# Performance work log

Hardware: AMD Instinct MI355X
Metric: run time of the kernel (lower is better)

Reference implementation:

```python
import jax, jax.numpy as jnp
import numpy as np

B, S, D = 4, 2048, 1024
H = 2 * D          # hidden_dim = 2*n_embd
A = H // 16        # adapt_dim
E = 8              # num_experts
GS = 4             # group_size
G = E // GS        # num_groups
K = 2              # top-k experts within group


def _ln(x, g, b, eps=1e-5):
    m = x.mean(-1, keepdims=True)
    v = ((x - m) ** 2).mean(-1, keepdims=True)
    return (x - m) * jax.lax.rsqrt(v + eps) * g + b


def setup_inputs() -> dict:
    key = jax.random.key(0)
    ks = jax.random.split(key, 14)
    n = lambda k, shape, s: jax.random.normal(k, shape, jnp.float32) * s
    sc = 1.0 / float(np.sqrt(D))
    asc = 0.01 / float(np.sqrt(A))
    return {
        'x': n(ks[0], (B, S, D), 1.0),
        'Wu': n(ks[1], (H, D), sc),        # shared_up
        'Wg': n(ks[2], (H, D), sc),        # shared_gate
        'Wd': n(ks[3], (D, H), sc),        # shared_down
        'Wpre': n(ks[4], (A, D), sc * 0.01),   # pre_adapt
        'Wpost': n(ks[5], (A, H), sc * 0.01),  # post_adapt
        'ln_g': jnp.ones((A,), jnp.float32),
        'ln_b': jnp.zeros((A,), jnp.float32),
        'Wap': n(ks[6], (H, A), sc * 0.01),    # adapt_proj
        'Wea': n(ks[7], (E, A, A), asc),       # per-expert adapter linears
        'ln_eg': jnp.ones((E, A), jnp.float32),
        'ln_eb': jnp.zeros((E, A), jnp.float32),
        'Wep': n(ks[8], (H, A), asc),          # expert_proj
        'Wop': n(ks[9], (D, H), asc),          # output_proj
        'Wgr': n(ks[10], (G, D), 0.001),       # router_group
        'Wer': n(ks[11], (GS, D), 0.001),      # router_expert
    }


def _forward(x, Wu, Wg, Wd, Wpre, Wpost, ln_g, ln_b, Wap, Wea, ln_eg, ln_eb, Wep, Wop, Wgr, Wer):
    N = B * S
    xf = x.reshape(N, D)
    # --- hierarchical router ---
    gl = xf @ Wgr.T                              # [N,G]
    gp = jax.nn.softmax(gl, axis=-1)
    gw, gi = jax.lax.top_k(gp, 1)                # top-1 group
    el = xf @ Wer.T                              # [N,GS]
    ep = jax.nn.softmax(el, axis=-1)
    lw, li = jax.lax.top_k(ep, K)                # top-k local experts
    lw = lw / (lw.sum(-1, keepdims=True) + 1e-7)
    fw = gw * lw                                 # [N,K] final weights
    idx = gi * GS + li                           # [N,K] global expert ids (distinct per token)
    dispatch = jnp.zeros((N, E), x.dtype).at[jnp.arange(N)[:, None], idx].set(fw)
    load = dispatch.sum(0)
    target = load.sum() / E
    rloss = 0.001 * (jnp.mean((load - target) ** 2) + jnp.mean(gl ** 2) + jnp.mean(el ** 2))
    # --- shared expert MLP ---
    hidden = jax.nn.silu(x @ Wg.T) * (x @ Wu.T)  # [B,S,H]
    ai = _ln(x @ Wpre.T, ln_g, ln_b)             # [B,S,A]
    ao = _ln(hidden @ Wpost.T, ln_g, ln_b)       # [B,S,A]
    aw = jax.nn.silu(jnp.clip(jnp.einsum('bsa,bta->bst', ai, ao), -5.0, 5.0))  # [B,S,S]
    adapt = jnp.einsum('bst,bta->bsa', aw, ai) @ Wap.T
    hidden = hidden + 0.1 * adapt
    shared = hidden @ Wd.T                       # [B,S,D]
    # --- expert group (dense form of masked gather/scatter; w==0 off-mask) ---
    w = dispatch.reshape(B, S, E)
    h0 = x @ Wpre.T                              # [B,S,A]
    he = _ln(jnp.einsum('bsa,eca->bsec', h0, Wea), ln_eg, ln_eb)  # [B,S,E,A]
    M = Wop @ Wep                                # output_proj o expert_proj, [D,A]
    out = shared * w.sum(-1, keepdims=True) + 0.1 * jnp.einsum('bsec,bse,dc->bsd', he, w, M)
    return out, rloss


def reference(x, Wu, Wg, Wd, Wpre, Wpost, ln_g, ln_b, Wap, Wea, ln_eg, ln_eb, Wep, Wop, Wgr, Wer):
    return _forward(x, Wu, Wg, Wd, Wpre, Wpost, ln_g, ln_b, Wap, Wea, ln_eg, ln_eb, Wep, Wop, Wgr, Wer)
```

## Files before the change

### kernel.cpp

```cpp
#include <hip/hip_runtime.h>
#include <math.h>


typedef __bf16 bf16_t;
typedef __attribute__((ext_vector_type(8))) __bf16 bf16x8;
typedef __attribute__((ext_vector_type(4))) float f32x4;

__device__ __forceinline__ float b2f(bf16_t v) { return (float)v; }
__device__ __forceinline__ bf16_t f2b(float v) { return (bf16_t)v; }
__device__ __forceinline__ float siluf(float v) { return v / (1.f + expf(-v)); }

static constexpr int Bb = 4, S = 2048, D = 1024, H = 2048, A = 128, E = 8;
static constexpr int N = Bb * S;

typedef __attribute__((address_space(1))) void gvoid;
typedef __attribute__((address_space(3))) void svoid;
__device__ __forceinline__ void gll16(const bf16_t* g, bf16_t* l) {
  __builtin_amdgcn_global_load_lds((gvoid*)g, (svoid*)l, 16, 0, 0);
}

__device__ __forceinline__ long tidx(int row, int k, int K, int lgTR) {
  int TRm = (1 << lgTR) - 1;
  int q = (k >> 3) & 3;
  int p = q ^ (row & 3);
  return ((((long)(row >> lgTR) * (K >> 5) + (k >> 5)) << lgTR) + (row & TRm)) * 32 +
         ((long)p << 3);
}

__device__ __forceinline__ bf16x8 ld8f(const float* p) {
  float4 a = *reinterpret_cast<const float4*>(p);
  float4 b = *reinterpret_cast<const float4*>(p + 4);
  bf16x8 r;
  r[0] = f2b(a.x); r[1] = f2b(a.y); r[2] = f2b(a.z); r[3] = f2b(a.w);
  r[4] = f2b(b.x); r[5] = f2b(b.y); r[6] = f2b(b.z); r[7] = f2b(b.w);
  return r;
}
__device__ __forceinline__ void split8(const float* p, bf16x8& h, bf16x8& l) {
  float4 a = *reinterpret_cast<const float4*>(p);
  float4 b = *reinterpret_cast<const float4*>(p + 4);
  float v[8] = {a.x, a.y, a.z, a.w, b.x, b.y, b.z, b.w};
#pragma unroll
  for (int j = 0; j < 8; j++) {
    bf16_t hh = f2b(v[j]);
    h[j] = hh;
    l[j] = f2b(v[j] - b2f(hh));
  }
}
__device__ __forceinline__ bf16x8 ld8m(const void* p, int row, int k, int K, int m) {
  if (m == 1) return ld8f(reinterpret_cast<const float*>(p) + (long)row * K + k);
  if (m == 2)
    return *reinterpret_cast<const bf16x8*>(
        reinterpret_cast<const bf16_t*>(p) + tidx(row, k, K, 7));
  return *reinterpret_cast<const bf16x8*>(
      reinterpret_cast<const bf16_t*>(p) + (long)row * K + k);
}

template <int LGTR, int LGNKS>
__global__ __launch_bounds__(256) void split_tiled(
    const float* __restrict__ in, bf16_t* __restrict__ hi,
    bf16_t* __restrict__ lo, long total, int K) {
  long stride = (long)gridDim.x * 256;
  for (long o = (long)blockIdx.x * 256 + threadIdx.x; o < total; o += stride) {
    int p = (int)(o & 3);
    long t = o >> 2;
    int r = (int)(t & ((1 << LGTR) - 1));
    long t2 = t >> LGTR;
    int ks = (int)(t2 & ((1 << LGNKS) - 1));
    long rt = t2 >> LGNKS;
    long row = (rt << LGTR) + r;
    int k = (ks << 5) + ((p ^ (r & 3)) << 3);
    bf16x8 h, l;
    split8(in + row * K + k, h, l);
    reinterpret_cast<bf16x8*>(hi)[o] = h;
    reinterpret_cast<bf16x8*>(lo)[o] = l;
  }
}

template <int WM, int WN, int MODE>
__global__ __launch_bounds__(256) void gemm_nt_b(
    const void* __restrict__ Ag, const void* __restrict__ Bg,
    void* __restrict__ Cv, void* __restrict__ Cv2, int M, int Nn, int K,
    const float* __restrict__ aux, int aF, int bF) {
  constexpr int BM = 2 * WM, BN = 2 * WN, AM = WM / 16, AN = WN / 16;
  constexpr int LDT = 40;
  __shared__ alignas(16) bf16_t As[BM * LDT];
  __shared__ alignas(16) bf16_t Bs[BN * LDT];

  const int tid = threadIdx.x;
  const int wave = tid >> 6, lane = tid & 63;
  const int wr = wave >> 1, wc = wave & 1;
  const int quad = lane >> 4, l16 = lane & 15;
  const int rowA0 = blockIdx.y * BM, rowB0 = blockIdx.x * BN;

  f32x4 acc[AM][AN] = {};

  for (int k0 = 0; k0 < K; k0 += 32) {
    for (int c = tid; c < BM * 4; c += 256) {
      int r = c >> 2, kc = c & 3;
      *reinterpret_cast<bf16x8*>(&As[r * LDT + kc * 8]) =
          ld8m(Ag, rowA0 + r, k0 + kc * 8, K, aF);
    }
    for (int c = tid; c < BN * 4; c += 256) {
      int r = c >> 2, kc = c & 3;
      *reinterpret_cast<bf16x8*>(&Bs[r * LDT + kc * 8]) =
          ld8m(Bg, rowB0 + r, k0 + kc * 8, K, bF);
    }
    __syncthreads();
    bf16x8 af[AM], bfv[AN];
#pragma unroll
    for (int i = 0; i < AM; i++)
      af[i] = *reinterpret_cast<bf16x8*>(&As[(wr * WM + i * 16 + l16) * LDT + quad * 8]);
#pragma unroll
    for (int j = 0; j < AN; j++)
      bfv[j] = *reinterpret_cast<bf16x8*>(&Bs[(wc * WN + j * 16 + l16) * LDT + quad * 8]);
#pragma unroll
    for (int i = 0; i < AM; i++)
#pragma unroll
      for (int j = 0; j < AN; j++)
        acc[i][j] = __builtin_amdgcn_mfma_f32_16x16x32_bf16(af[i], bfv[j], acc[i][j], 0, 0, 0);
    __syncthreads();
  }

#pragma unroll
  for (int i = 0; i < AM; i++)
#pragma unroll
    for (int j = 0; j < AN; j++)
#pragma unroll
      for (int r = 0; r < 4; r++) {
        int row = rowA0 + wr * WM + i * 16 + quad * 4 + r;
        int col = rowB0 + wc * WN + j * 16 + l16;
        float v = acc[i][j][r];
        if constexpr (MODE == 0) {
          reinterpret_cast<bf16_t*>(Cv)[(long)row * Nn + col] = f2b(v);
        } else if constexpr (MODE == 1) {
          v = fminf(fmaxf(v, -5.f), 5.f);
          reinterpret_cast<bf16_t*>(Cv)[(long)row * Nn + col] = f2b(siluf(v));
        } else if constexpr (MODE == 2) {
          float* C = reinterpret_cast<float*>(Cv);
          long o = (long)row * Nn + col;
          C[o] = C[o] + 0.1f * v;
        } else if constexpr (MODE == 3) {
          float* C = reinterpret_cast<float*>(Cv);
          long o = (long)row * Nn + col;
          C[o] = C[o] * aux[row] + 0.1f * v;
        } else {
          bf16_t* Ch = reinterpret_cast<bf16_t*>(Cv);
          bf16_t* Cl = reinterpret_cast<bf16_t*>(Cv2);
          long o = tidx(row, col, Nn, 7) + (col & 7);
          float s = b2f(Ch[o]) + b2f(Cl[o]) + 0.1f * v;
          bf16_t hh = f2b(s);
          Ch[o] = hh;
          Cl[o] = f2b(s - b2f(hh));
        }
      }
}

__global__ __launch_bounds__(256) void gemm_gu_g(
    const bf16_t* __restrict__ xhT, const bf16_t* __restrict__ xlT,
    const bf16_t* __restrict__ WghT, const bf16_t* __restrict__ WglT,
    const bf16_t* __restrict__ WuhT, const bf16_t* __restrict__ WulT,
    bf16_t* __restrict__ Hh, bf16_t* __restrict__ Hl) {
  __shared__ alignas(16) bf16_t Ah[128 * 32];
  __shared__ alignas(16) bf16_t Al[128 * 32];
  __shared__ alignas(16) bf16_t B1h[64 * 32];
  __shared__ alignas(16) bf16_t B1l[64 * 32];
  __shared__ alignas(16) bf16_t B2h[64 * 32];
  __shared__ alignas(16) bf16_t B2l[64 * 32];

  const int tid = threadIdx.x;
  const int wave = tid >> 6, lane = tid & 63;
  const int wr = wave >> 1, wc = wave & 1;
  const int quad = lane >> 4, l16 = lane & 15;
  const int sw = (quad ^ (l16 & 3)) << 3;
  const int bm = blockIdx.y, bn = blockIdx.x;
  constexpr int nks = D / 32;

  f32x4 ag[4][2] = {}, au[4][2] = {};

  for (int ks = 0; ks < nks; ks++) {
    const int wo = wave << 9;
    long ao = (((long)bm * nks + ks) << 12) + wo + lane * 8;
    long bo = (((long)bn * nks + ks) << 11) + wo + lane * 8;
    gll16(xhT + ao, Ah + wo);
    gll16(xhT + ao + 2048, Ah + wo + 2048);
    gll16(xlT + ao, Al + wo);
    gll16(xlT + ao + 2048, Al + wo + 2048);
    gll16(WghT + bo, B1h + wo);
    gll16(WglT + bo, B1l + wo);
    gll16(WuhT + bo, B2h + wo);
    gll16(WulT + bo, B2l + wo);
    __syncthreads();
    bf16x8 afh[4], afl[4], b1h[2], b1l[2], b2h[2], b2l[2];
#pragma unroll
    for (int i = 0; i < 4; i++) {
      int ro = (wr * 64 + i * 16 + l16) * 32 + sw;
      afh[i] = *reinterpret_cast<bf16x8*>(&Ah[ro]);
      afl[i] = *reinterpret_cast<bf16x8*>(&Al[ro]);
    }
#pragma unroll
    for (int j = 0; j < 2; j++) {
      int ro = (wc * 32 + j * 16 + l16) * 32 + sw;
      b1h[j] = *reinterpret_cast<bf16x8*>(&B1h[ro]);
      b1l[j] = *reinterpret_cast<bf16x8*>(&B1l[ro]);
      b2h[j] = *reinterpret_cast<bf16x8*>(&B2h[ro]);
      b2l[j] = *reinterpret_cast<bf16x8*>(&B2l[ro]);
    }
#pragma unroll
    for (int i = 0; i < 4; i++)
#pragma unroll
      for (int j = 0; j < 2; j++) {
        ag[i][j] = __builtin_amdgcn_mfma_f32_16x16x32_bf16(afh[i], b1h[j], ag[i][j], 0, 0, 0);
        ag[i][j] = __builtin_amdgcn_mfma_f32_16x16x32_bf16(afh[i], b1l[j], ag[i][j], 0, 0, 0);
        ag[i][j] = __builtin_amdgcn_mfma_f32_16x16x32_bf16(afl[i], b1h[j], ag[i][j], 0, 0, 0);
        au[i][j] = __builtin_amdgcn_mfma_f32_16x16x32_bf16(afh[i], b2h[j], au[i][j], 0, 0, 0);
        au[i][j] = __builtin_amdgcn_mfma_f32_16x16x32_bf16(afh[i], b2l[j], au[i][j], 0, 0, 0);
        au[i][j] = __builtin_amdgcn_mfma_f32_16x16x32_bf16(afl[i], b2h[j], au[i][j], 0, 0, 0);
      }
    __syncthreads();
  }

#pragma unroll
  for (int i = 0; i < 4; i++)
#pragma unroll
    for (int j = 0; j < 2; j++)
#pragma unroll
      for (int r = 0; r < 4; r++) {
        int row = bm * 128 + wr * 64 + i * 16 + quad * 4 + r;
        int col = bn * 64 + wc * 32 + j * 16 + l16;
        long o = tidx(row, col, H, 7) + (col & 7);
        float v = siluf(ag[i][j][r]) * au[i][j][r];
        bf16_t hh = f2b(v);
        Hh[o] = hh;
        Hl[o] = f2b(v - b2f(hh));
      }
}

__global__ __launch_bounds__(256) void gemm_dn_g(
    const bf16_t* __restrict__ HhT, const bf16_t* __restrict__ HlT,
    const bf16_t* __restrict__ WdhT, const bf16_t* __restrict__ WdlT,
    float* __restrict__ Cg) {
  __shared__ alignas(16) bf16_t Ah[128 * 32];
  __shared__ alignas(16) bf16_t Al[128 * 32];
  __shared__ alignas(16) bf16_t Bh[128 * 32];
  __shared__ alignas(16) bf16_t Bl[128 * 32];

  const int tid = threadIdx.x;
  const int wave = tid >> 6, lane = tid & 63;
  const int wr = wave >> 1, wc = wave & 1;
  const int quad = lane >> 4, l16 = lane & 15;
  const int sw = (quad ^ (l16 & 3)) << 3;
  const int by = blockIdx.y, bx = blockIdx.x;
  constexpr int nks = H / 32;

  f32x4 acc[4][4] = {};

  for (int ks = 0; ks < nks; ks++) {
    const int wo = wave << 9;
    long ao = (((long)by * nks + ks) << 12) + wo + lane * 8;
    long bo = (((long)bx * nks + ks) << 12) + wo + lane * 8;
    gll16(HhT + ao, Ah + wo);
    gll16(HhT + ao + 2048, Ah + wo + 2048);
    gll16(HlT + ao, Al + wo);
    gll16(HlT + ao + 2048, Al + wo + 2048);
    gll16(WdhT + bo, Bh + wo);
    gll16(WdhT + bo + 2048, Bh + wo + 2048);
    gll16(WdlT + bo, Bl + wo);
    gll16(WdlT + bo + 2048, Bl + wo + 2048);
    __syncthreads();
    bf16x8 afh[4], afl[4], bfh[4], bfl[4];
#pragma unroll
    for (int i = 0; i < 4; i++) {
      int ro = (wr * 64 + i * 16 + l16) * 32 + sw;
      afh[i] = *reinterpret_cast<bf16x8*>(&Ah[ro]);
      afl[i] = *reinterpret_cast<bf16x8*>(&Al[ro]);
    }
#pragma unroll
    for (int j = 0; j < 4; j++) {
      int ro = (wc * 64 + j * 16 + l16) * 32 + sw;
      bfh[j] = *reinterpret_cast<bf16x8*>(&Bh[ro]);
      bfl[j] = *reinterpret_cast<bf16x8*>(&Bl[ro]);
    }
#pragma unroll
    for (int i = 0; i < 4; i++)
#pragma unroll
      for (int j = 0; j < 4; j++) {
        acc[i][j] = __builtin_amdgcn_mfma_f32_16x16x32_bf16(afh[i], bfh[j], acc[i][j], 0, 0, 0);
        acc[i][j] = __builtin_amdgcn_mfma_f32_16x16x32_bf16(afh[i], bfl[j], acc[i][j], 0, 0, 0);
        acc[i][j] = __builtin_amdgcn_mfma_f32_16x16x32_bf16(afl[i], bfh[j], acc[i][j], 0, 0, 0);
      }
    __syncthreads();
  }

#pragma unroll
  for (int i = 0; i < 4; i++)
#pragma unroll
    for (int j = 0; j < 4; j++)
#pragma unroll
      for (int r = 0; r < 4; r++) {
        int row = by * 128 + wr * 64 + i * 16 + quad * 4 + r;
        int col = bx * 128 + wc * 64 + j * 16 + l16;
        Cg[(long)row * D + col] = acc[i][j][r];
      }
}

__global__ __launch_bounds__(256) void fused_adapt(
    const bf16_t* __restrict__ aib, const bf16_t* __restrict__ aob,
    const bf16_t* __restrict__ aiT, bf16_t* __restrict__ adpre) {
  constexpr int LDQ = 136;
  constexpr int LDP = 72;
  __shared__ alignas(16) bf16_t Qs[64 * LDQ];
  __shared__ alignas(16) bf16_t Os[64 * LDQ];
  __shared__ alignas(16) bf16_t Ps[64 * LDP];
  __shared__ alignas(16) bf16_t Vs[128 * LDP];

  const int tid = threadIdx.x;
  const int wave = tid >> 6, lane = tid & 63;
  const int wr = wave >> 1, wc = wave & 1;
  const int quad = lane >> 4, l16 = lane & 15;
  const int b = blockIdx.y;
  const int q0 = blockIdx.x * 64;

  for (int c = tid; c < 1024; c += 256) {
    int r = c >> 4, cc = c & 15;
    *reinterpret_cast<bf16x8*>(&Qs[r * LDQ + cc * 8]) =
        *reinterpret_cast<const bf16x8*>(&aib[((long)b * S + q0 + r) * A + cc * 8]);
  }

  f32x4 o[2][4] = {};

  for (int tt = 0; tt < S / 64; tt++) {
    const int t0 = tt * 64;
    __syncthreads();
    for (int c = tid; c < 1024; c += 256) {
      int r = c >> 4, cc = c & 15;
      *reinterpret_cast<bf16x8*>(&Os[r * LDQ + cc * 8]) =
          *reinterpret_cast<const bf16x8*>(&aob[((long)b * S + t0 + r) * A + cc * 8]);
    }
    for (int c = tid; c < 1024; c += 256) {
      int r = c >> 3, cc = c & 7;
      *reinterpret_cast<bf16x8*>(&Vs[r * LDP + cc * 8]) =
          *reinterpret_cast<const bf16x8*>(&aiT[((long)b * A + r) * S + t0 + cc * 8]);
    }
    __syncthreads();
    f32x4 p[2][2] = {};
#pragma unroll
    for (int ks = 0; ks < 4; ks++) {
      bf16x8 af[2], bfv[2];
#pragma unroll
      for (int i = 0; i < 2; i++)
        af[i] = *reinterpret_cast<bf16x8*>(&Qs[(wr * 32 + i * 16 + l16) * LDQ + ks * 32 + quad * 8]);
#pragma unroll
      for (int j = 0; j < 2; j++)
        bfv[j] = *reinterpret_cast<bf16x8*>(&Os[(wc * 32 + j * 16 + l16) * LDQ + ks * 32 + quad * 8]);
#pragma unroll
      for (int i = 0; i < 2; i++)
#pragma unroll
        for (int j = 0; j < 2; j++)
          p[i][j] = __builtin_amdgcn_mfma_f32_16x16x32_bf16(af[i], bfv[j], p[i][j], 0, 0, 0);
    }
#pragma unroll
    for (int i = 0; i < 2; i++)
#pragma unroll
      for (int j = 0; j < 2; j++)
#pragma unroll
        for (int r = 0; r < 4; r++) {
          int row = wr * 32 + i * 16 + quad * 4 + r;
          int col = wc * 32 + j * 16 + l16;
          float v = fminf(fmaxf(p[i][j][r], -5.f), 5.f);
          Ps[row * LDP + col] = f2b(siluf(v));
        }
    __syncthreads();
#pragma unroll
    for (int ks = 0; ks < 2; ks++) {
      bf16x8 paf[2], vbf[4];
#pragma unroll
      for (int i = 0; i < 2; i++)
        paf[i] = *reinterpret_cast<bf16x8*>(&Ps[(wr * 32 + i * 16 + l16) * LDP + ks * 32 + quad * 8]);
#pragma unroll
      for (int j = 0; j < 4; j++)
        vbf[j] = *reinterpret_cast<bf16x8*>(&Vs[(wc * 64 + j * 16 + l16) * LDP + ks * 32 + quad * 8]);
#pragma unroll
      for (int i = 0; i < 2; i++)
#pragma unroll
        for (int j = 0; j < 4; j++)
          o[i][j] = __builtin_amdgcn_mfma_f32_16x16x32_bf16(paf[i], vbf[j], o[i][j], 0, 0, 0);
    }
  }

#pragma unroll
  for (int i = 0; i < 2; i++)
#pragma unroll
    for (int j = 0; j < 4; j++)
#pragma unroll
      for (int r = 0; r < 4; r++) {
        int row = q0 + wr * 32 + i * 16 + quad * 4 + r;
        int col = wc * 64 + j * 16 + l16;
        adpre[((long)b * S + row) * A + col] = f2b(o[i][j][r]);
      }
}

__global__ __launch_bounds__(256) void gemm_mb_splitk(
    const float* __restrict__ Ag, const bf16_t* __restrict__ Bg,
    float* __restrict__ Mp, int M, int Nn, int K) {
  constexpr int BM = 64, BN = 64, LDT = 40;
  __shared__ alignas(16) bf16_t As[BM * LDT];
  __shared__ alignas(16) bf16_t Bs[BN * LDT];
  const int tid = threadIdx.x;
  const int wave = tid >> 6, lane = tid & 63;
  const int wr = wave >> 1, wc = wave & 1;
  const int quad = lane >> 4, l16 = lane & 15;
  const int rowA0 = blockIdx.y * BM, rowB0 = blockIdx.x * BN;
  const int kz = blockIdx.z;
  const int ks0 = kz * (K / 8), ks1 = ks0 + K / 8;

  f32x4 acc[2][2] = {};
  for (int k0 = ks0; k0 < ks1; k0 += 32) {
    for (int c = tid; c < BM * 4; c += 256) {
      int r = c >> 2, kc = c & 3;
      *reinterpret_cast<bf16x8*>(&As[r * LDT + kc * 8]) =
          ld8f(Ag + (long)(rowA0 + r) * K + k0 + kc * 8);
    }
    for (int c = tid; c < BN * 4; c += 256) {
      int r = c >> 2, kc = c & 3;
      *reinterpret_cast<bf16x8*>(&Bs[r * LDT + kc * 8]) =
          *reinterpret_cast<const bf16x8*>(&Bg[(long)(rowB0 + r) * K + k0 + kc * 8]);
    }
    __syncthreads();
    bf16x8 af[2], bfv[2];
#pragma unroll
    for (int i = 0; i < 2; i++)
      af[i] = *reinterpret_cast<bf16x8*>(&As[(wr * 32 + i * 16 + l16) * LDT + quad * 8]);
#pragma unroll
    for (int j = 0; j < 2; j++)
      bfv[j] = *reinterpret_cast<bf16x8*>(&Bs[(wc * 32 + j * 16 + l16) * LDT + quad * 8]);
#pragma unroll
    for (int i = 0; i < 2; i++)
#pragma unroll
      for (int j = 0; j < 2; j++)
        acc[i][j] = __builtin_amdgcn_mfma_f32_16x16x32_bf16(af[i], bfv[j], acc[i][j], 0, 0, 0);
    __syncthreads();
  }
#pragma unroll
  for (int i = 0; i < 2; i++)
#pragma unroll
    for (int j = 0; j < 2; j++)
#pragma unroll
      for (int r = 0; r < 4; r++) {
        int row = rowA0 + wr * 32 + i * 16 + quad * 4 + r;
        int col = rowB0 + wc * 32 + j * 16 + l16;
        Mp[(long)kz * M * Nn + (long)row * Nn + col] = acc[i][j][r];
      }
}

__global__ __launch_bounds__(256) void mb_combine(
    const float* __restrict__ Mp, bf16_t* __restrict__ Mb, int total) {
  int i = blockIdx.x * 256 + threadIdx.x;
  if (i >= total) return;
  float s = 0.f;
#pragma unroll
  for (int z = 0; z < 8; z++) s += Mp[(long)z * total + i];
  Mb[i] = f2b(s);
}

__global__ __launch_bounds__(256) void gemm_dn_hl(
    const float* __restrict__ Ag, const float* __restrict__ Bg,
    float* __restrict__ Cg, int M, int Nn, int K) {
  constexpr int BM = 128, BN = 128, LDT = 40;
  __shared__ alignas(16) bf16_t Ah[BM * LDT];
  __shared__ alignas(16) bf16_t Al[BM * LDT];
  __shared__ alignas(16) bf16_t Bh[BN * LDT];
  __shared__ alignas(16) bf16_t Bl[BN * LDT];

  const int tid = threadIdx.x;
  const int wave = tid >> 6, lane = tid & 63;
  const int wr = wave >> 1, wc = wave & 1;
  const int quad = lane >> 4, l16 = lane & 15;
  const int rowA0 = blockIdx.y * BM, rowB0 = blockIdx.x * BN;

  f32x4 acc[4][4] = {};

  for (int k0 = 0; k0 < K; k0 += 32) {
    for (int c = tid; c < BM * 4; c += 256) {
      int r = c >> 2, kc = c & 3;
      bf16x8 h, l;
      split8(&Ag[(long)(rowA0 + r) * K + k0 + kc * 8], h, l);
      *reinterpret_cast<bf16x8*>(&Ah[r * LDT + kc * 8]) = h;
      *reinterpret_cast<bf16x8*>(&Al[r * LDT + kc * 8]) = l;
    }
    for (int c = tid; c < BN * 4; c += 256) {
      int r = c >> 2, kc = c & 3;
      bf16x8 h, l;
      split8(&Bg[(long)(rowB0 + r) * K + k0 + kc * 8], h, l);
      *reinterpret_cast<bf16x8*>(&Bh[r * LDT + kc * 8]) = h;
      *reinterpret_cast<bf16x8*>(&Bl[r * LDT + kc * 8]) = l;
    }
    __syncthreads();
    bf16x8 afh[4], afl[4], bfh[4], bfl[4];
#pragma unroll
    for (int i = 0; i < 4; i++) {
      int ro = (wr * 64 + i * 16 + l16) * LDT + quad * 8;
      afh[i] = *reinterpret_cast<bf16x8*>(&Ah[ro]);
      afl[i] = *reinterpret_cast<bf16x8*>(&Al[ro]);
    }
#pragma unroll
    for (int j = 0; j < 4; j++) {
      int ro = (wc * 64 + j * 16 + l16) * LDT + quad * 8;
      bfh[j] = *reinterpret_cast<bf16x8*>(&Bh[ro]);
      bfl[j] = *reinterpret_cast<bf16x8*>(&Bl[ro]);
    }
#pragma unroll
    for (int i = 0; i < 4; i++)
#pragma unroll
      for (int j = 0; j < 4; j++) {
        acc[i][j] = __builtin_amdgcn_mfma_f32_16x16x32_bf16(afh[i], bfh[j], acc[i][j], 0, 0, 0);
        acc[i][j] = __builtin_amdgcn_mfma_f32_16x16x32_bf16(afh[i], bfl[j], acc[i][j], 0, 0, 0);
        acc[i][j] = __builtin_amdgcn_mfma_f32_16x16x32_bf16(afl[i], bfh[j], acc[i][j], 0, 0, 0);
      }
    __syncthreads();
  }

#pragma unroll
  for (int i = 0; i < 4; i++)
#pragma unroll
    for (int j = 0; j < 4; j++)
#pragma unroll
      for (int r = 0; r < 4; r++) {
        int row = rowA0 + wr * 64 + i * 16 + quad * 4 + r;
        int col = rowB0 + wc * 64 + j * 16 + l16;
        Cg[(long)row * Nn + col] = acc[i][j][r];
      }
}

__global__ __launch_bounds__(256) void gemm_gu_hl(
    const float* __restrict__ x, const float* __restrict__ Wg,
    const float* __restrict__ Wu, float* __restrict__ Cg, int M, int Nn, int K) {
  constexpr int BM = 128, BN = 64, LDT = 40;
  __shared__ alignas(16) bf16_t Ah[BM * LDT];
  __shared__ alignas(16) bf16_t Al[BM * LDT];
  __shared__ alignas(16) bf16_t B1h[BN * LDT];
  __shared__ alignas(16) bf16_t B1l[BN * LDT];
  __shared__ alignas(16) bf16_t B2h[BN * LDT];
  __shared__ alignas(16) bf16_t B2l[BN * LDT];

  const int tid = threadIdx.x;
// ... 95 lines not shown
    float mg = fmaxf(gl0, gl1);
    float e0 = expf(gl0 - mg), e1 = expf(gl1 - mg);
    float inv = 1.f / (e0 + e1);
    float gp0 = e0 * inv, gp1 = e1 * inv;
    int gi = (gp1 > gp0) ? 1 : 0;
    float gw = gi ? gp1 : gp0;
    float el[4] = {dots[2], dots[3], dots[4], dots[5]};
    float me = fmaxf(fmaxf(el[0], el[1]), fmaxf(el[2], el[3]));
    float ep[4], es = 0.f;
#pragma unroll
    for (int j = 0; j < 4; j++) { ep[j] = expf(el[j] - me); es += ep[j]; }
    float inve = 1.f / es;
#pragma unroll
    for (int j = 0; j < 4; j++) ep[j] *= inve;
    int i1 = 0;
    for (int j = 1; j < 4; j++) if (ep[j] > ep[i1]) i1 = j;
    int i2 = (i1 == 0) ? 1 : 0;
    for (int j = 0; j < 4; j++) if (j != i1 && j != i2 && ep[j] > ep[i2]) i2 = j;
    float l1 = ep[i1], l2 = ep[i2];
    float ils = 1.f / (l1 + l2 + 1e-7f);
    float f1 = gw * l1 * ils, f2 = gw * l2 * ils;
    eidx[token * 2] = gi * 4 + i1;
    eidx[token * 2 + 1] = gi * 4 + i2;
    fw[token * 2] = f1;
    fw[token * 2 + 1] = f2;
    wsum[token] = f1 + f2;
    part[wv][gi * 4 + i1] = f1;
    part[wv][gi * 4 + i2] = f2;
    part[wv][8] = gl0 * gl0 + gl1 * gl1;
    part[wv][9] = el[0] * el[0] + el[1] * el[1] + el[2] * el[2] + el[3] * el[3];
  }
  __syncthreads();
  if (threadIdx.x < 12) {
    lpart[(long)blockIdx.x * 12 + threadIdx.x] =
        part[0][threadIdx.x] + part[1][threadIdx.x] +
        part[2][threadIdx.x] + part[3][threadIdx.x];
  }
}

__global__ __launch_bounds__(256) void ln_rows(
    const bf16_t* __restrict__ in, const float* __restrict__ g,
    const float* __restrict__ b, bf16_t* __restrict__ out) {
  const int row = blockIdx.x * 4 + (threadIdx.x >> 6);
  const int lane = threadIdx.x & 63;
  const bf16_t* p = in + (long)row * A;
  float x0 = b2f(p[lane]), x1 = b2f(p[lane + 64]);
  float s = x0 + x1;
#pragma unroll
  for (int off = 32; off; off >>= 1) s += __shfl_xor(s, off);
  float mean = s * (1.f / 128.f);
  float d0 = x0 - mean, d1 = x1 - mean;
  float q = d0 * d0 + d1 * d1;
#pragma unroll
  for (int off = 32; off; off >>= 1) q += __shfl_xor(q, off);
  float r = rsqrtf(q * (1.f / 128.f) + 1e-5f);
  bf16_t* po = out + (long)row * A;
  po[lane] = f2b(d0 * r * g[lane] + b[lane]);
  po[lane + 64] = f2b(d1 * r * g[lane + 64] + b[lane + 64]);
}

__global__ __launch_bounds__(256) void transpose2d(
    const void* __restrict__ in, bf16_t* __restrict__ out, int R, int C, int isf) {
  __shared__ bf16_t t[32][33];
  const long zb = blockIdx.z;
  const long ib = zb * (long)R * C;
  bf16_t* op = out + zb * (long)R * C;
  const int r0 = blockIdx.y * 32, c0 = blockIdx.x * 32;
  const int tx = threadIdx.x & 31, ty = threadIdx.x >> 5;
#pragma unroll
  for (int i = 0; i < 4; i++) {
    long idx = ib + (long)(r0 + ty + i * 8) * C + c0 + tx;
    t[ty + i * 8][tx] = isf ? f2b(reinterpret_cast<const float*>(in)[idx])
                            : reinterpret_cast<const bf16_t*>(in)[idx];
  }
  __syncthreads();
#pragma unroll
  for (int i = 0; i < 4; i++) op[(long)(c0 + ty + i * 8) * R + r0 + tx] = t[tx][ty + i * 8];
}

__global__ __launch_bounds__(128) void expert_adapt(
    const bf16_t* __restrict__ h0, const bf16_t* __restrict__ WeaT,
    const float* __restrict__ ln_eg, const float* __restrict__ ln_eb,
    const int* __restrict__ eidx, const float* __restrict__ fw,
    bf16_t* __restrict__ hw) {
  const int n = blockIdx.x;
  const int c = threadIdx.x;
  __shared__ float h0s[128];
  __shared__ float red[4];
  h0s[c] = b2f(h0[(long)n * A + c]);
  __syncthreads();
  float out = 0.f;
  for (int k = 0; k < 2; k++) {
    int e = eidx[n * 2 + k];
    e = min(max(e, 0), E - 1);
    float w = fw[n * 2 + k];
    const bf16_t* Wc = WeaT + (long)e * A * A + c;
    float t = 0.f;
#pragma unroll 8
    for (int a = 0; a < 128; a++) t += b2f(Wc[(long)a * A]) * h0s[a];
    float s = t, q = t * t;
#pragma unroll
    for (int off = 32; off; off >>= 1) { s += __shfl_xor(s, off); q += __shfl_xor(q, off); }
    if ((c & 63) == 0) { red[(c >> 6) * 2] = s; red[(c >> 6) * 2 + 1] = q; }
    __syncthreads();
    float Sx = red[0] + red[2], Qx = red[1] + red[3];
    float mean = Sx * (1.f / 128.f);
    float var = Qx * (1.f / 128.f) - mean * mean;
    float r = rsqrtf(var + 1e-5f);
    out += w * ((t - mean) * r * ln_eg[e * A + c] + ln_eb[e * A + c]);
    __syncthreads();
  }
  hw[(long)n * A + c] = f2b(out);
}

__global__ __launch_bounds__(256) void finalize_loss(
    const float* __restrict__ lpart, int nblk, float* __restrict__ outv) {
  float acc[10] = {};
  for (int b = threadIdx.x; b < nblk; b += 256) {
    const float* p = lpart + (long)b * 12;
#pragma unroll
    for (int c = 0; c < 10; c++) acc[c] += p[c];
  }
  __shared__ float red[10][4];
  const int lane = threadIdx.x & 63, wv = threadIdx.x >> 6;
#pragma unroll
  for (int c = 0; c < 10; c++) {
    float s = acc[c];
#pragma unroll
    for (int off = 32; off; off >>= 1) s += __shfl_xor(s, off);
    if (lane == 0) red[c][wv] = s;
  }
  __syncthreads();
  if (threadIdx.x == 0) {
    float loss[10];
#pragma unroll
    for (int c = 0; c < 10; c++)
      loss[c] = red[c][0] + red[c][1] + red[c][2] + red[c][3];
    float tl = 0.f;
    for (int e = 0; e < 8; e++) tl += loss[e];
    float target = tl / 8.f;
    float mse = 0.f;
    for (int e = 0; e < 8; e++) { float d = loss[e] - target; mse += d * d; }
    mse *= (1.f / 8.f);
    outv[0] = 0.001f * (mse + loss[8] / (float)(N * 2) + loss[9] / (float)(N * 4));
  }
}

extern "C" void kernel_launch(void* const* d_in, const int* in_sizes, int n_in,
                              void* d_out, int out_size, void* d_ws, size_t ws_size,
                              hipStream_t stream) {
  const float* x = (const float*)d_in[0];
  const float* Wu = (const float*)d_in[1];
  const float* Wg = (const float*)d_in[2];
  const float* Wd = (const float*)d_in[3];
  const float* Wpre = (const float*)d_in[4];
  const float* Wpost = (const float*)d_in[5];
  const float* ln_g = (const float*)d_in[6];
  const float* ln_b = (const float*)d_in[7];
  const float* Wap = (const float*)d_in[8];
  const float* Wea = (const float*)d_in[9];
  const float* ln_eg = (const float*)d_in[10];
  const float* ln_eb = (const float*)d_in[11];
  const float* Wep = (const float*)d_in[12];
  const float* Wop = (const float*)d_in[13];
  const float* Wgr = (const float*)d_in[14];
  const float* Wer = (const float*)d_in[15];
  float* out = (float*)d_out;

  char* ws = (char*)d_ws;
  size_t off = 0;
  auto alloc = [&](size_t bytes) { char* p = ws + off; off += (bytes + 255) & ~size_t(255); return p; };
  float* lpart = (float*)alloc((size_t)(N / 4) * 12 * 4);
  float* wsum = (float*)alloc((size_t)N * 4);
  float* fwb = (float*)alloc((size_t)N * 2 * 4);
  int* eidx = (int*)alloc((size_t)N * 2 * 4);
  bf16_t* Mb = (bf16_t*)alloc((size_t)D * A * 2);
  float* Mp = (float*)alloc((size_t)8 * D * A * 4);
  bf16_t* WepT = (bf16_t*)alloc((size_t)H * A * 2);
  bf16_t* hwb = (bf16_t*)alloc((size_t)N * A * 2);
  bf16_t* h0b = (bf16_t*)alloc((size_t)N * A * 2);
  bf16_t* aib = (bf16_t*)alloc((size_t)N * A * 2);
  bf16_t* scrA = (bf16_t*)alloc((size_t)N * A * 2);
  bf16_t* aob = (bf16_t*)alloc((size_t)N * A * 2);
  bf16_t* adpreb = (bf16_t*)alloc((size_t)N * A * 2);
  bf16_t* WeaT = (bf16_t*)alloc((size_t)E * A * A * 2);
  bf16_t* aopre = scrA;
  bf16_t* aiT = scrA;

  const bool big = ws_size >= ((size_t)140 << 20);
  float* hiddenF = nullptr;
  bf16_t *xh = nullptr, *xl = nullptr;
  bf16_t *Wgh = nullptr, *Wgl = nullptr, *Wuh = nullptr, *Wul = nullptr;
  bf16_t *Wdh = nullptr, *Wdl = nullptr, *Hh = nullptr, *Hl = nullptr;
  if (big) {
    xh = (bf16_t*)alloc((size_t)N * D * 2);
    xl = (bf16_t*)alloc((size_t)N * D * 2);
    Wgh = (bf16_t*)alloc((size_t)H * D * 2);
    Wgl = (bf16_t*)alloc((size_t)H * D * 2);
    Wuh = (bf16_t*)alloc((size_t)H * D * 2);
    Wul = (bf16_t*)alloc((size_t)H * D * 2);
    Wdh = (bf16_t*)alloc((size_t)D * H * 2);
    Wdl = (bf16_t*)alloc((size_t)D * H * 2);
    Hh = (bf16_t*)alloc((size_t)N * H * 2);
    Hl = (bf16_t*)alloc((size_t)N * H * 2);
  } else {
    hiddenF = (float*)alloc((size_t)N * H * 4);
  }
  (void)ws_size; (void)in_sizes; (void)n_in; (void)out_size;

  const dim3 blk(256);

  router_kernel<<<dim3(N / 4), blk, 0, stream>>>(x, Wgr, Wer, eidx, fwb, wsum, lpart);
  transpose2d<<<dim3(A / 32, A / 32, E), blk, 0, stream>>>(Wea, WeaT, A, A, 1);

  if (big) {
    split_tiled<7, 5><<<dim3(2048), blk, 0, stream>>>(x, xh, xl, (long)N * D / 8, D);
    split_tiled<6, 5><<<dim3(512), blk, 0, stream>>>(Wg, Wgh, Wgl, (long)H * D / 8, D);
    split_tiled<6, 5><<<dim3(512), blk, 0, stream>>>(Wu, Wuh, Wul, (long)H * D / 8, D);
    split_tiled<7, 6><<<dim3(512), blk, 0, stream>>>(Wd, Wdh, Wdl, (long)D * H / 8, H);
    gemm_gu_g<<<dim3(H / 64, N / 128), blk, 0, stream>>>(
        xh, xl, Wgh, Wgl, Wuh, Wul, Hh, Hl);
    gemm_nt_b<16, 32, 0><<<dim3(A / 64, N / 32), blk, 0, stream>>>(
        xh, Wpre, h0b, nullptr, N, A, D, nullptr, 2, 1);
    ln_rows<<<dim3(N / 4), blk, 0, stream>>>(h0b, ln_g, ln_b, aib);
    gemm_nt_b<16, 32, 0><<<dim3(A / 64, N / 32), blk, 0, stream>>>(
        Hh, Wpost, aopre, nullptr, N, A, H, nullptr, 2, 1);
    ln_rows<<<dim3(N / 4), blk, 0, stream>>>(aopre, ln_g, ln_b, aob);
    transpose2d<<<dim3(A / 32, S / 32, Bb), blk, 0, stream>>>(aib, aiT, S, A, 0);
    fused_adapt<<<dim3(S / 64, Bb), blk, 0, stream>>>(aib, aob, aiT, adpreb);
    gemm_nt_b<64, 64, 4><<<dim3(H / 128, N / 128), blk, 0, stream>>>(
        adpreb, Wap, Hh, Hl, N, H, A, nullptr, 0, 1);
    gemm_dn_g<<<dim3(D / 128, N / 128), blk, 0, stream>>>(Hh, Hl, Wdh, Wdl, out);
  } else {
    gemm_gu_hl<<<dim3(H / 64, N / 128), blk, 0, stream>>>(x, Wg, Wu, hiddenF, N, H, D);
    gemm_nt_b<16, 32, 0><<<dim3(A / 64, N / 32), blk, 0, stream>>>(
        x, Wpre, h0b, nullptr, N, A, D, nullptr, 1, 1);
    ln_rows<<<dim3(N / 4), blk, 0, stream>>>(h0b, ln_g, ln_b, aib);
    gemm_nt_b<16, 32, 0><<<dim3(A / 64, N / 32), blk, 0, stream>>>(
        hiddenF, Wpost, aopre, nullptr, N, A, H, nullptr, 1, 1);
    ln_rows<<<dim3(N / 4), blk, 0, stream>>>(aopre, ln_g, ln_b, aob);
    transpose2d<<<dim3(A / 32, S / 32, Bb), blk, 0, stream>>>(aib, aiT, S, A, 0);
    fused_adapt<<<dim3(S / 64, Bb), blk, 0, stream>>>(aib, aob, aiT, adpreb);
    gemm_nt_b<64, 64, 2><<<dim3(H / 128, N / 128), blk, 0, stream>>>(
        adpreb, Wap, hiddenF, nullptr, N, H, A, nullptr, 0, 1);
    gemm_dn_hl<<<dim3(D / 128, N / 128), blk, 0, stream>>>(hiddenF, Wd, out, N, D, H);
  }

  transpose2d<<<dim3(A / 32, H / 32, 1), blk, 0, stream>>>(Wep, WepT, H, A, 1);
  gemm_mb_splitk<<<dim3(A / 64, D / 64, 8), blk, 0, stream>>>(
      Wop, WepT, Mp, D, A, H);
  mb_combine<<<dim3((D * A + 255) / 256), blk, 0, stream>>>(Mp, Mb, D * A);
  expert_adapt<<<dim3(N), dim3(128), 0, stream>>>(h0b, WeaT, ln_eg, ln_eb, eidx, fwb, hwb);
  gemm_nt_b<64, 64, 3><<<dim3(D / 128, N / 128), blk, 0, stream>>>(
      hwb, Mb, out, nullptr, N, D, A, wsum, 0, 0);
  finalize_loss<<<dim3(1), blk, 0, stream>>>(lpart, N / 4, out + (size_t)N * D);
}
```

Measured before the change: 790.0 us.

## Fold adapt projection into final GEMM via Wd·Wap and double-buffer split GEMMs

Rather than adding 0.1*adapt@Wap^T into the hi/lo hidden split before the down projection, the adapt term is folded algebraically. The code precomputes Wd·Wap^T as a [D,A] matrix and concatenates it with Wop·Wep into a K=256 operand. fused_adapt writes the wsum-scaled adapt output into the second half of the expert activation buffer, so a single final GEMM handles both terms and the H-wide read-modify-write GEMM is dropped. gemm_gu_g and gemm_dn_g gain LDS double buffering with prefetch of the next k-slice and a changed swizzle pattern. The cost is a bf16 rounding of the combined Wd·Wap matrix, which is a precision risk, and doubled LDS use that may cut occupancy.

Result: slower. 807.9 us (+2.3%).

```diff
diff --git a/kernel.cpp b/kernel.cpp
--- a/kernel.cpp
+++ b/kernel.cpp
@@ -22,7 +22,7 @@
 __device__ __forceinline__ long tidx(int row, int k, int K, int lgTR) {
   int TRm = (1 << lgTR) - 1;
   int q = (k >> 3) & 3;
-  int p = q ^ (row & 3);
+  int p = q ^ ((row >> 1) & 3);
   return ((((long)(row >> lgTR) * (K >> 5) + (k >> 5)) << lgTR) + (row & TRm)) * 32 +
          ((long)p << 3);
 }
@@ -68,7 +68,7 @@
     int ks = (int)(t2 & ((1 << LGNKS) - 1));
     long rt = t2 >> LGNKS;
     long row = (rt << LGTR) + r;
-    int k = (ks << 5) + ((p ^ (r & 3)) << 3);
+    int k = (ks << 5) + ((p ^ ((r >> 1) & 3)) << 3);
     bf16x8 h, l;
     split8(in + row * K + k, h, l);
     reinterpret_cast<bf16x8*>(hi)[o] = h;
@@ -79,7 +79,7 @@
 template <int WM, int WN, int MODE>
 __global__ __launch_bounds__(256) void gemm_nt_b(
     const void* __restrict__ Ag, const void* __restrict__ Bg,
-    void* __restrict__ Cv, void* __restrict__ Cv2, int M, int Nn, int K,
+    void* __restrict__ Cv, int M, int Nn, int K,
     const float* __restrict__ aux, int aF, int bF) {
   constexpr int BM = 2 * WM, BN = 2 * WN, AM = WM / 16, AN = WN / 16;
   constexpr int LDT = 40;
@@ -129,28 +129,19 @@
       for (int r = 0; r < 4; r++) {
         int row = rowA0 + wr * WM + i * 16 + quad * 4 + r;
         int col = rowB0 + wc * WN + j * 16 + l16;
+        long o = (long)row * Nn + col;
         float v = acc[i][j][r];
         if constexpr (MODE == 0) {
-          reinterpret_cast<bf16_t*>(Cv)[(long)row * Nn + col] = f2b(v);
+          reinterpret_cast<bf16_t*>(Cv)[o] = f2b(v);
         } else if constexpr (MODE == 1) {
           v = fminf(fmaxf(v, -5.f), 5.f);
-          reinterpret_cast<bf16_t*>(Cv)[(long)row * Nn + col] = f2b(siluf(v));
+          reinterpret_cast<bf16_t*>(Cv)[o] = f2b(siluf(v));
         } else if constexpr (MODE == 2) {
           float* C = reinterpret_cast<float*>(Cv);
-          long o = (long)row * Nn + col;
           C[o] = C[o] + 0.1f * v;
-        } else if constexpr (MODE == 3) {
+        } else {
           float* C = reinterpret_cast<float*>(Cv);
-          long o = (long)row * Nn + col;
           C[o] = C[o] * aux[row] + 0.1f * v;
-        } else {
-          bf16_t* Ch = reinterpret_cast<bf16_t*>(Cv);
-          bf16_t* Cl = reinterpret_cast<bf16_t*>(Cv2);
-          long o = tidx(row, col, Nn, 7) + (col & 7);
-          float s = b2f(Ch[o]) + b2f(Cl[o]) + 0.1f * v;
-          bf16_t hh = f2b(s);
-          Ch[o] = hh;
-          Cl[o] = f2b(s - b2f(hh));
         }
       }
 }
@@ -160,50 +151,56 @@
     const bf16_t* __restrict__ WghT, const bf16_t* __restrict__ WglT,
     const bf16_t* __restrict__ WuhT, const bf16_t* __restrict__ WulT,
     bf16_t* __restrict__ Hh, bf16_t* __restrict__ Hl) {
-  __shared__ alignas(16) bf16_t Ah[128 * 32];
-  __shared__ alignas(16) bf16_t Al[128 * 32];
-  __shared__ alignas(16) bf16_t B1h[64 * 32];
-  __shared__ alignas(16) bf16_t B1l[64 * 32];
-  __shared__ alignas(16) bf16_t B2h[64 * 32];
-  __shared__ alignas(16) bf16_t B2l[64 * 32];
+  __shared__ alignas(16) bf16_t Ah[2][128 * 32];
+  __shared__ alignas(16) bf16_t Al[2][128 * 32];
+  __shared__ alignas(16) bf16_t B1h[2][64 * 32];
+  __shared__ alignas(16) bf16_t B1l[2][64 * 32];
+  __shared__ alignas(16) bf16_t B2h[2][64 * 32];
+  __shared__ alignas(16) bf16_t B2l[2][64 * 32];
 
   const int tid = threadIdx.x;
   const int wave = tid >> 6, lane = tid & 63;
   const int wr = wave >> 1, wc = wave & 1;
   const int quad = lane >> 4, l16 = lane & 15;
-  const int sw = (quad ^ (l16 & 3)) << 3;
+  const int sw = (quad ^ ((l16 >> 1) & 3)) << 3;
   const int bm = blockIdx.y, bn = blockIdx.x;
   constexpr int nks = D / 32;
-
-  f32x4 ag[4][2] = {}, au[4][2] = {};
-
-  for (int ks = 0; ks < nks; ks++) {
-    const int wo = wave << 9;
+  const int wo = wave << 9;
+
+  auto stage = [&](int buf, int ks) {
     long ao = (((long)bm * nks + ks) << 12) + wo + lane * 8;
     long bo = (((long)bn * nks + ks) << 11) + wo + lane * 8;
-    gll16(xhT + ao, Ah + wo);
-    gll16(xhT + ao + 2048, Ah + wo + 2048);
-    gll16(xlT + ao, Al + wo);
-    gll16(xlT + ao + 2048, Al + wo + 2048);
-    gll16(WghT + bo, B1h + wo);
-    gll16(WglT + bo, B1l + wo);
-    gll16(WuhT + bo, B2h + wo);
-    gll16(WulT + bo, B2l + wo);
-    __syncthreads();
+    gll16(xhT + ao, &Ah[buf][wo]);
+    gll16(xhT + ao + 2048, &Ah[buf][wo + 2048]);
+    gll16(xlT + ao, &Al[buf][wo]);
+    gll16(xlT + ao + 2048, &Al[buf][wo + 2048]);
+    gll16(WghT + bo, &B1h[buf][wo]);
+    gll16(WglT + bo, &B1l[buf][wo]);
+    gll16(WuhT + bo, &B2h[buf][wo]);
+    gll16(WulT + bo, &B2l[buf][wo]);
+  };
+
+  f32x4 ag[4][2] = {}, au[4][2] = {};
+
+  stage(0, 0);
+  __syncthreads();
+  int cur = 0;
+  for (int ks = 0; ks < nks; ks++) {
+    if (ks + 1 < nks) stage(cur ^ 1, ks + 1);
     bf16x8 afh[4], afl[4], b1h[2], b1l[2], b2h[2], b2l[2];
 #pragma unroll
     for (int i = 0; i < 4; i++) {
       int ro = (wr * 64 + i * 16 + l16) * 32 + sw;
-      afh[i] = *reinterpret_cast<bf16x8*>(&Ah[ro]);
-      afl[i] = *reinterpret_cast<bf16x8*>(&Al[ro]);
+      afh[i] = *reinterpret_cast<bf16x8*>(&Ah[cur][ro]);
+      afl[i] = *reinterpret_cast<bf16x8*>(&Al[cur][ro]);
     }
 #pragma unroll
     for (int j = 0; j < 2; j++) {
       int ro = (wc * 32 + j * 16 + l16) * 32 + sw;
-      b1h[j] = *reinterpret_cast<bf16x8*>(&B1h[ro]);
-      b1l[j] = *reinterpret_cast<bf16x8*>(&B1l[ro]);
-      b2h[j] = *reinterpret_cast<bf16x8*>(&B2h[ro]);
-      b2l[j] = *reinterpret_cast<bf16x8*>(&B2l[ro]);
+      b1h[j] = *reinterpret_cast<bf16x8*>(&B1h[cur][ro]);
+      b1l[j] = *reinterpret_cast<bf16x8*>(&B1l[cur][ro]);
+      b2h[j] = *reinterpret_cast<bf16x8*>(&B2h[cur][ro]);
+      b2l[j] = *reinterpret_cast<bf16x8*>(&B2l[cur][ro]);
     }
 #pragma unroll
     for (int i = 0; i < 4; i++)
@@ -217,6 +214,7 @@
         au[i][j] = __builtin_amdgcn_mfma_f32_16x16x32_bf16(afl[i], b2h[j], au[i][j], 0, 0, 0);
       }
     __syncthreads();
+    cur ^= 1;
   }
 
 #pragma unroll
@@ -239,46 +237,52 @@
     const bf16_t* __restrict__ HhT, const bf16_t* __restrict__ HlT,
     const bf16_t* __restrict__ WdhT, const bf16_t* __restrict__ WdlT,
     float* __restrict__ Cg) {
-  __shared__ alignas(16) bf16_t Ah[128 * 32];
-  __shared__ alignas(16) bf16_t Al[128 * 32];
-  __shared__ alignas(16) bf16_t Bh[128 * 32];
-  __shared__ alignas(16) bf16_t Bl[128 * 32];
+  __shared__ alignas(16) bf16_t Ah[2][128 * 32];
+  __shared__ alignas(16) bf16_t Al[2][128 * 32];
+  __shared__ alignas(16) bf16_t Bh[2][128 * 32];
+  __shared__ alignas(16) bf16_t Bl[2][128 * 32];
 
   const int tid = threadIdx.x;
   const int wave = tid >> 6, lane = tid & 63;
   const int wr = wave >> 1, wc = wave & 1;
   const int quad = lane >> 4, l16 = lane & 15;
-  const int sw = (quad ^ (l16 & 3)) << 3;
+  const int sw = (quad ^ ((l16 >> 1) & 3)) << 3;
   const int by = blockIdx.y, bx = blockIdx.x;
   constexpr int nks = H / 32;
-
-  f32x4 acc[4][4] = {};
-
-  for (int ks = 0; ks < nks; ks++) {
-    const int wo = wave << 9;
+  const int wo = wave << 9;
+
+  auto stage = [&](int buf, int ks) {
     long ao = (((long)by * nks + ks) << 12) + wo + lane * 8;
     long bo = (((long)bx * nks + ks) << 12) + wo + lane * 8;
-    gll16(HhT + ao, Ah + wo);
-    gll16(HhT + ao + 2048, Ah + wo + 2048);
-    gll16(HlT + ao, Al + wo);
-    gll16(HlT + ao + 2048, Al + wo + 2048);
-    gll16(WdhT + bo, Bh + wo);
-    gll16(WdhT + bo + 2048, Bh + wo + 2048);
-    gll16(WdlT + bo, Bl + wo);
-    gll16(WdlT + bo + 2048, Bl + wo + 2048);
-    __syncthreads();
+    gll16(HhT + ao, &Ah[buf][wo]);
+    gll16(HhT + ao + 2048, &Ah[buf][wo + 2048]);
+    gll16(HlT + ao, &Al[buf][wo]);
+    gll16(HlT + ao + 2048, &Al[buf][wo + 2048]);
+    gll16(WdhT + bo, &Bh[buf][wo]);
+    gll16(WdhT + bo + 2048, &Bh[buf][wo + 2048]);
+    gll16(WdlT + bo, &Bl[buf][wo]);
+    gll16(WdlT + bo + 2048, &Bl[buf][wo + 2048]);
+  };
+
+  f32x4 acc[4][4] = {};
+
+  stage(0, 0);
+  __syncthreads();
+  int cur = 0;
+  for (int ks = 0; ks < nks; ks++) {
+    if (ks + 1 < nks) stage(cur ^ 1, ks + 1);
     bf16x8 afh[4], afl[4], bfh[4], bfl[4];
 #pragma unroll
     for (int i = 0; i < 4; i++) {
       int ro = (wr * 64 + i * 16 + l16) * 32 + sw;
-      afh[i] = *reinterpret_cast<bf16x8*>(&Ah[ro]);
-      afl[i] = *reinterpret_cast<bf16x8*>(&Al[ro]);
+      afh[i] = *reinterpret_cast<bf16x8*>(&Ah[cur][ro]);
+      afl[i] = *reinterpret_cast<bf16x8*>(&Al[cur][ro]);
     }
 #pragma unroll
     for (int j = 0; j < 4; j++) {
       int ro = (wc * 64 + j * 16 + l16) * 32 + sw;
-      bfh[j] = *reinterpret_cast<bf16x8*>(&Bh[ro]);
-      bfl[j] = *reinterpret_cast<bf16x8*>(&Bl[ro]);
+      bfh[j] = *reinterpret_cast<bf16x8*>(&Bh[cur][ro]);
+      bfl[j] = *reinterpret_cast<bf16x8*>(&Bl[cur][ro]);
     }
 #pragma unroll
     for (int i = 0; i < 4; i++)
@@ -289,6 +293,7 @@
         acc[i][j] = __builtin_amdgcn_mfma_f32_16x16x32_bf16(afl[i], bfh[j], acc[i][j], 0, 0, 0);
       }
     __syncthreads();
+    cur ^= 1;
   }
 
 #pragma unroll
@@ -305,7 +310,8 @@
 
 __global__ __launch_bounds__(256) void fused_adapt(
     const bf16_t* __restrict__ aib, const bf16_t* __restrict__ aob,
-    const bf16_t* __restrict__ aiT, bf16_t* __restrict__ adpre) {
+    const bf16_t* __restrict__ aiT, bf16_t* __restrict__ outp,
+    int oLd, int oOff, const float* __restrict__ wsum) {
   constexpr int LDQ = 136;
   constexpr int LDP = 72;
   __shared__ alignas(16) bf16_t Qs[64 * LDQ];
@@ -395,7 +401,9 @@
       for (int r = 0; r < 4; r++) {
         int row = q0 + wr * 32 + i * 16 + quad * 4 + r;
         int col = wc * 64 + j * 16 + l16;
-        adpre[((long)b * S + row) * A + col] = f2b(o[i][j][r]);
+        long token = (long)b * S + row;
+        float sc = wsum ? wsum[token] : 1.f;
+        outp[token * oLd + oOff + col] = f2b(o[i][j][r] * sc);
       }
 }
 
@@ -453,13 +461,14 @@
 }
 
 __global__ __launch_bounds__(256) void mb_combine(
-    const float* __restrict__ Mp, bf16_t* __restrict__ Mb, int total) {
+    const float* __restrict__ Mp, bf16_t* __restrict__ outp, int total,
+    int ld, int coff) {
   int i = blockIdx.x * 256 + threadIdx.x;
   if (i >= total) return;
   float s = 0.f;
 #pragma unroll
   for (int z = 0; z < 8; z++) s += Mp[(long)z * total + i];
-  Mb[i] = f2b(s);
+  outp[(long)(i >> 7) * ld + coff + (i & 127)] = f2b(s);
 }
 
 __global__ __launch_bounds__(256) void gemm_dn_hl(
@@ -721,7 +730,7 @@
     const bf16_t* __restrict__ h0, const bf16_t* __restrict__ WeaT,
     const float* __restrict__ ln_eg, const float* __restrict__ ln_eb,
     const int* __restrict__ eidx, const float* __restrict__ fw,
-    bf16_t* __restrict__ hw) {
+    bf16_t* __restrict__ hw, int ld) {
   const int n = blockIdx.x;
   const int c = threadIdx.x;
   __shared__ float h0s[128];
@@ -749,7 +758,7 @@
     out += w * ((t - mean) * r * ln_eg[e * A + c] + ln_eb[e * A + c]);
     __syncthreads();
   }
-  hw[(long)n * A + c] = f2b(out);
+  hw[(long)n * ld + c] = f2b(out);
 }
 
 __global__ __launch_bounds__(256) void finalize_loss(
@@ -813,15 +822,15 @@
   float* wsum = (float*)alloc((size_t)N * 4);
   float* fwb = (float*)alloc((size_t)N * 2 * 4);
   int* eidx = (int*)alloc((size_t)N * 2 * 4);
-  bf16_t* Mb = (bf16_t*)alloc((size_t)D * A * 2);
+  bf16_t* Mb2 = (bf16_t*)alloc((size_t)D * 256 * 2);
   float* Mp = (float*)alloc((size_t)8 * D * A * 4);
   bf16_t* WepT = (bf16_t*)alloc((size_t)H * A * 2);
-  bf16_t* hwb = (bf16_t*)alloc((size_t)N * A * 2);
+  bf16_t* WapT = (bf16_t*)alloc((size_t)H * A * 2);
+  bf16_t* hw2 = (bf16_t*)alloc((size_t)N * 256 * 2);
   bf16_t* h0b = (bf16_t*)alloc((size_t)N * A * 2);
   bf16_t* aib = (bf16_t*)alloc((size_t)N * A * 2);
   bf16_t* scrA = (bf16_t*)alloc((size_t)N * A * 2);
   bf16_t* aob = (bf16_t*)alloc((size_t)N * A * 2);
-  bf16_t* adpreb = (bf16_t*)alloc((size_t)N * A * 2);
   bf16_t* WeaT = (bf16_t*)alloc((size_t)E * A * A * 2);
   bf16_t* aopre = scrA;
   bf16_t* aiT = scrA;
@@ -860,37 +869,48 @@
     gemm_gu_g<<<dim3(H / 64, N / 128), blk, 0, stream>>>(
         xh, xl, Wgh, Wgl, Wuh, Wul, Hh, Hl);
     gemm_nt_b<16, 32, 0><<<dim3(A / 64, N / 32), blk, 0, stream>>>(
-        xh, Wpre, h0b, nullptr, N, A, D, nullptr, 2, 1);
+        xh, Wpre, h0b, N, A, D, nullptr, 2, 1);
     ln_rows<<<dim3(N / 4), blk, 0, stream>>>(h0b, ln_g, ln_b, aib);
     gemm_nt_b<16, 32, 0><<<dim3(A / 64, N / 32), blk, 0, stream>>>(
-        Hh, Wpost, aopre, nullptr, N, A, H, nullptr, 2, 1);
+        Hh, Wpost, aopre, N, A, H, nullptr, 2, 1);
     ln_rows<<<dim3(N / 4), blk, 0, stream>>>(aopre, ln_g, ln_b, aob);
     transpose2d<<<dim3(A / 32, S / 32, Bb), blk, 0, stream>>>(aib, aiT, S, A, 0);
-    fused_adapt<<<dim3(S / 64, Bb), blk, 0, stream>>>(aib, aob, aiT, adpreb);
-    gemm_nt_b<64, 64, 4><<<dim3(H / 128, N / 128), blk, 0, stream>>>(
-        adpreb, Wap, Hh, Hl, N, H, A, nullptr, 0, 1);
+    fused_adapt<<<dim3(S / 64, Bb), blk, 0, stream>>>(
+        aib, aob, aiT, hw2, 256, 128, wsum);
     gemm_dn_g<<<dim3(D / 128, N / 128), blk, 0, stream>>>(Hh, Hl, Wdh, Wdl, out);
+    transpose2d<<<dim3(A / 32, H / 32, 1), blk, 0, stream>>>(Wep, WepT, H, A, 1);
+    transpose2d<<<dim3(A / 32, H / 32, 1), blk, 0, stream>>>(Wap, WapT, H, A, 1);
+    gemm_mb_splitk<<<dim3(A / 64, D / 64, 8), blk, 0, stream>>>(Wop, WepT, Mp, D, A, H);
+    mb_combine<<<dim3((D * A + 255) / 256), blk, 0, stream>>>(Mp, Mb2, D * A, 256, 0);
+    gemm_mb_splitk<<<dim3(A / 64, D / 64, 8), blk, 0, stream>>>(Wd, WapT, Mp, D, A, H);
+    mb_combine<<<dim3((D * A + 255) / 256), blk, 0, stream>>>(Mp, Mb2, D * A, 256, 128);
+    expert_adapt<<<dim3(N), dim3(128), 0, stream>>>(
+        h0b, WeaT, ln_eg, ln_eb, eidx, fwb, hw2, 256);
+    gemm_nt_b<64, 64, 3><<<dim3(D / 128, N / 128), blk, 0, stream>>>(
+        hw2, Mb2, out, N, D, 256, wsum, 0, 0);
   } else {
+    bf16_t* adpreb = hw2 + (size_t)N * A;
     gemm_gu_hl<<<dim3(H / 64, N / 128), blk, 0, stream>>>(x, Wg, Wu, hiddenF, N, H, D);
     gemm_nt_b<16, 32, 0><<<dim3(A / 64, N / 32), blk, 0, stream>>>(
-        x, Wpre, h0b, nullptr, N, A, D, nullptr, 1, 1);
+        x, Wpre, h0b, N, A, D, nullptr, 1, 1);
     ln_rows<<<dim3(N / 4), blk, 0, stream>>>(h0b, ln_g, ln_b, aib);
     gemm_nt_b<16, 32, 0><<<dim3(A / 64, N / 32), blk, 0, stream>>>(
-        hiddenF, Wpost, aopre, nullptr, N, A, H, nullptr, 1, 1);
+        hiddenF, Wpost, aopre, N, A, H, nullptr, 1, 1);
     ln_rows<<<dim3(N / 4), blk, 0, stream>>>(aopre, ln_g, ln_b, aob);
     transpose2d<<<dim3(A / 32, S / 32, Bb), blk, 0, stream>>>(aib, aiT, S, A, 0);
-    fused_adapt<<<dim3(S / 64, Bb), blk, 0, stream>>>(aib, aob, aiT, adpreb);
+    fused_adapt<<<dim3(S / 64, Bb), blk, 0, stream>>>(
+        aib, aob, aiT, adpreb, 128, 0, nullptr);
     gemm_nt_b<64, 64, 2><<<dim3(H / 128, N / 128), blk, 0, stream>>>(
-        adpreb, Wap, hiddenF, nullptr, N, H, A, nullptr, 0, 1);
+        adpreb, Wap, hiddenF, N, H, A, nullptr, 0, 1);
     gemm_dn_hl<<<dim3(D / 128, N / 128), blk, 0, stream>>>(hiddenF, Wd, out, N, D, H);
-  }
-
-  transpose2d<<<dim3(A / 32, H / 32, 1), blk, 0, stream>>>(Wep, WepT, H, A, 1);
-  gemm_mb_splitk<<<dim3(A / 64, D / 64, 8), blk, 0, stream>>>(
-      Wop, WepT, Mp, D, A, H);
-  mb_combine<<<dim3((D * A + 255) / 256), blk, 0, stream>>>(Mp, Mb, D * A);
-  expert_adapt<<<dim3(N), dim3(128), 0, stream>>>(h0b, WeaT, ln_eg, ln_eb, eidx, fwb, hwb);
-  gemm_nt_b<64, 64, 3><<<dim3(D / 128, N / 128), blk, 0, stream>>>(
-      hwb, Mb, out, nullptr, N, D, A, wsum, 0, 0);
+    transpose2d<<<dim3(A / 32, H / 32, 1), blk, 0, stream>>>(Wep, WepT, H, A, 1);
+    gemm_mb_splitk<<<dim3(A / 64, D / 64, 8), blk, 0, stream>>>(Wop, WepT, Mp, D, A, H);
+    mb_combine<<<dim3((D * A + 255) / 256), blk, 0, stream>>>(Mp, Mb2, D * A, 128, 0);
+    expert_adapt<<<dim3(N), dim3(128), 0, stream>>>(
+        h0b, WeaT, ln_eg, ln_eb, eidx, fwb, hw2, 128);
+    gemm_nt_b<64, 64, 3><<<dim3(D / 128, N / 128), blk, 0, stream>>>(
+        hw2, Mb2, out, N, D, A, wsum, 0, 0);
+  }
+
   finalize_loss<<<dim3(1), blk, 0, stream>>>(lpart, N / 4, out + (size_t)N * D);
 }
```
